# Kernel optimization log

Hardware: AMD Instinct MI355X
Metric: run time of the kernel (lower is better)

Reference implementation:

```python
import jax, jax.numpy as jnp
import numpy as np

# Config from VoVNetBEVTransformer: D=41, C=128, downsample=16, final_dim=(128,352)
B, N, C = 4, 6, 128
D, FH, FW = 41, 8, 22
OGH, OGW = 128, 352
XB = (-50.0, 50.0, 0.5)
YB = (-50.0, 50.0, 0.5)
ZB = (-10.0, 10.0, 20.0)
DBOUND = (4.0, 45.0, 1.0)
NX = int((XB[1] - XB[0]) / XB[2])  # 200
NY = int((YB[1] - YB[0]) / YB[2])  # 200
NZ = int((ZB[1] - ZB[0]) / ZB[2])  # 1


def _grid():
    dx = jnp.array([XB[2], YB[2], ZB[2]], jnp.float32)
    bx = jnp.array([XB[0] + XB[2] / 2.0, YB[0] + YB[2] / 2.0, ZB[0] + ZB[2] / 2.0], jnp.float32)
    return dx, bx


def _frustum():
    # (D, FH, FW, 3) grid of (u_pixel, v_pixel, depth) as in create_frustum
    ds = jnp.arange(DBOUND[0], DBOUND[1], DBOUND[2], dtype=jnp.float32)
    xs = jnp.linspace(0.0, OGW - 1.0, FW, dtype=jnp.float32)
    ys = jnp.linspace(0.0, OGH - 1.0, FH, dtype=jnp.float32)
    ds = jnp.broadcast_to(ds[:, None, None], (D, FH, FW))
    xs = jnp.broadcast_to(xs[None, None, :], (D, FH, FW))
    ys = jnp.broadcast_to(ys[None, :, None], (D, FH, FW))
    return jnp.stack([xs, ys, ds], axis=-1)


def setup_inputs() -> dict:
    key = jax.random.key(0)
    ks = jax.random.split(key, 6)
    cam_feats = jax.random.normal(ks[0], (B, N, D, FH, FW, C), jnp.float32)
    # cam-to-ego rotation: camera z (forward) -> ego x, plus small perturbation
    Rbase = jnp.array([[0.0, 0.0, 1.0], [-1.0, 0.0, 0.0], [0.0, -1.0, 0.0]], jnp.float32)
    rots = Rbase[None, None] + 0.02 * jax.random.normal(ks[1], (B, N, 3, 3), jnp.float32)
    trans = 1.5 * jax.random.normal(ks[2], (B, N, 3), jnp.float32)
    K = jnp.array([[500.0, 0.0, 176.0], [0.0, 500.0, 64.0], [0.0, 0.0, 1.0]], jnp.float32)
    intrins = K[None, None] + 0.5 * jax.random.normal(ks[3], (B, N, 3, 3), jnp.float32)
    post_rots = jnp.eye(3, dtype=jnp.float32)[None, None] + 0.01 * jax.random.normal(ks[4], (B, N, 3, 3), jnp.float32)
    post_trans = 0.5 * jax.random.normal(ks[5], (B, N, 3), jnp.float32)
    return {"cam_feats": cam_feats, "rots": rots, "trans": trans, "intrins": intrins,
            "post_rots": post_rots, "post_trans": post_trans}


def reference(cam_feats, rots, trans, intrins, post_rots, post_trans):
    dx, bx = _grid()
    frustum = _frustum()  # (D,FH,FW,3)
    # --- get_geometry ---
    pts = frustum[None, None] - post_trans[:, :, None, None, None, :]          # (B,N,D,FH,FW,3)
    pts = jnp.einsum('bnij,bndhwj->bndhwi', jnp.linalg.inv(post_rots), pts)
    pts = jnp.concatenate([pts[..., :2] * pts[..., 2:3], pts[..., 2:3]], axis=-1)
    combine = rots @ jnp.linalg.inv(intrins)
    pts = jnp.einsum('bnij,bndhwj->bndhwi', combine, pts) + trans[:, :, None, None, None, :]
    # --- voxel_pooling (QuickCumsum == segment-sum over voxel ranks) ---
    x = cam_feats.reshape(-1, C)                                               # (Nprime, C)
    g = ((pts - (bx - dx / 2.0)) / dx).astype(jnp.int32).reshape(-1, 3)        # trunc like torch .long()
    b_ix = jnp.repeat(jnp.arange(B, dtype=jnp.int32), N * D * FH * FW)
    kept = ((g[:, 0] >= 0) & (g[:, 0] < NX) & (g[:, 1] >= 0) & (g[:, 1] < NY)
            & (g[:, 2] >= 0) & (g[:, 2] < NZ))
    gc = jnp.clip(g, 0, jnp.array([NX - 1, NY - 1, NZ - 1], jnp.int32))
    S = NX * NY * NZ * B
    seg = ((gc[:, 0] * NY + gc[:, 1]) * NZ + gc[:, 2]) * B + b_ix              # same rank formula
    seg = jnp.where(kept, seg, S)                                              # dummy bin for dropped pts
    pooled = jax.ops.segment_sum(x, seg, num_segments=S + 1)[:S]               # (S, C)
    final = pooled.reshape(NX, NY, NZ, B, C).transpose(3, 2, 4, 0, 1)          # (B,NZ,C,NX,NY)
    return final.reshape(B, NZ * C, NX, NY)                                    # cat along z -> channels
```

## Files before the change

kernel.cpp:

```cpp
#include <hip/hip_runtime.h>

#define BATCH 4
#define NCAM  6
#define DNUM  41
#define FHN   8
#define FWN   22
#define CCH   128
#define NXV   200
#define NYV   200
#define NXY   40000
#define NPTS  173184

struct Mats {
    float iR[9];
    float comb[9];
    float tr[3];
    float pt[3];
};

__device__ void inv3x3_f32_gesv(const float* __restrict__ Ain, float* __restrict__ inv) {
#pragma clang fp contract(off)
    float A[9];
    for (int k = 0; k < 9; ++k) A[k] = Ain[k];
    int piv[3];
    for (int j = 0; j < 3; ++j) {
        int p = j;
        float amax = fabsf(A[j * 3 + j]);
        for (int i = j + 1; i < 3; ++i) {
            float v = fabsf(A[i * 3 + j]);
            if (v > amax) { amax = v; p = i; }
        }
        piv[j] = p;
        if (p != j)
            for (int k = 0; k < 3; ++k) { float t = A[j*3+k]; A[j*3+k] = A[p*3+k]; A[p*3+k] = t; }
        float rd = 1.0f / A[j * 3 + j];
        for (int i = j + 1; i < 3; ++i) A[i * 3 + j] = A[i * 3 + j] * rd;
        for (int i = j + 1; i < 3; ++i)
            for (int k = j + 1; k < 3; ++k)
                A[i * 3 + k] = A[i * 3 + k] - A[i * 3 + j] * A[j * 3 + k];
    }
    float rdiag[3] = {1.0f / A[0], 1.0f / A[4], 1.0f / A[8]};
    for (int c = 0; c < 3; ++c) {
        float b[3] = {0.0f, 0.0f, 0.0f};
        b[c] = 1.0f;
        for (int j = 0; j < 3; ++j) { int p = piv[j]; if (p != j) { float t = b[j]; b[j] = b[p]; b[p] = t; } }
        for (int k = 0; k < 3; ++k)
            for (int i = k + 1; i < 3; ++i)
                b[i] = b[i] - A[i * 3 + k] * b[k];
        for (int k = 2; k >= 0; --k) {
            b[k] = b[k] * rdiag[k];
            for (int i = 0; i < k; ++i)
                b[i] = b[i] - A[i * 3 + k] * b[k];
        }
        inv[0 + c] = b[0];
        inv[3 + c] = b[1];
        inv[6 + c] = b[2];
    }
}

__global__ void prep_kernel(const float* __restrict__ rots,
                            const float* __restrict__ trans,
                            const float* __restrict__ intrins,
                            const float* __restrict__ post_rots,
                            const float* __restrict__ post_trans,
                            Mats* __restrict__ mats) {
    int i = threadIdx.x;
    if (i >= BATCH * NCAM) return;
    Mats m;
    inv3x3_f32_gesv(post_rots + i * 9, m.iR);
    float invK[9];
    inv3x3_f32_gesv(intrins + i * 9, invK);
    {
#pragma clang fp contract(off)
        for (int r = 0; r < 3; ++r)
            for (int c = 0; c < 3; ++c) {
                float s = rots[i * 9 + r * 3 + 0] * invK[0 * 3 + c];
                s = s + rots[i * 9 + r * 3 + 1] * invK[1 * 3 + c];
                s = s + rots[i * 9 + r * 3 + 2] * invK[2 * 3 + c];
                m.comb[r * 3 + c] = s;
            }
    }
    for (int k = 0; k < 3; ++k) {
        m.tr[k] = trans[i * 3 + k];
        m.pt[k] = post_trans[i * 3 + k];
    }
    mats[i] = m;
}

__device__ __forceinline__ int point_voxel(int p, const Mats* __restrict__ mats) {
#pragma clang fp contract(off)
    int w = p % FWN;
    int t = p / FWN;
    int h = t % FHN;
    t /= FHN;
    int d = t % DNUM;
    t /= DNUM;
    int n = t % NCAM;
    int b = t / NCAM;

    const Mats m = mats[b * NCAM + n];

    float u   = (float)((double)w * (351.0 / 21.0));
    float v   = (float)((double)h * (127.0 / 7.0));
    float dep = 4.0f + (float)d;

    float p0 = u - m.pt[0];
    float p1 = v - m.pt[1];
    float p2 = dep - m.pt[2];
    float q0 = m.iR[0] * p0; q0 = q0 + m.iR[1] * p1; q0 = q0 + m.iR[2] * p2;
    float q1 = m.iR[3] * p0; q1 = q1 + m.iR[4] * p1; q1 = q1 + m.iR[5] * p2;
    float q2 = m.iR[6] * p0; q2 = q2 + m.iR[7] * p1; q2 = q2 + m.iR[8] * p2;
    float r0 = q0 * q2;
    float r1 = q1 * q2;
    float e0 = m.comb[0] * r0; e0 = e0 + m.comb[1] * r1; e0 = e0 + m.comb[2] * q2; e0 = e0 + m.tr[0];
    float e1 = m.comb[3] * r0; e1 = e1 + m.comb[4] * r1; e1 = e1 + m.comb[5] * q2; e1 = e1 + m.tr[1];
    float e2 = m.comb[6] * r0; e2 = e2 + m.comb[7] * r1; e2 = e2 + m.comb[8] * q2; e2 = e2 + m.tr[2];

    float gxf = (e0 + 50.0f) / 0.5f;
    float gyf = (e1 + 50.0f) / 0.5f;
    float gzf = (e2 + 10.0f) / 20.0f;
    int gx = (int)gxf;
    int gy = (int)gyf;
    int gz = (int)gzf;
    if (gx < 0 || gx >= NXV || gy < 0 || gy >= NYV || gz < 0 || gz >= 1) return -1;
    return b * NXY + gx * NYV + gy;
}

__global__ __launch_bounds__(128) void scatter_vox_kernel(const float* __restrict__ feats,
                                                          const Mats* __restrict__ mats,
                                                          float* __restrict__ vox) {
    int p = blockIdx.x;
    int vid = point_voxel(p, mats);
    if (vid < 0) return;
    int c = threadIdx.x;
    float f = feats[(size_t)p * CCH + c];
    atomicAdd(vox + (size_t)vid * CCH + c, f);
}

__global__ __launch_bounds__(256) void transpose_kernel(const float* __restrict__ vox,
                                                        float* __restrict__ out) {
    __shared__ float tile[32][33];
    int xy0 = blockIdx.x * 32;
    int c0  = blockIdx.y * 32;
    int b   = blockIdx.z;
    int tx = threadIdx.x, ty = threadIdx.y;
    const float* src = vox + (size_t)b * NXY * CCH;
#pragma unroll
    for (int j = 0; j < 32; j += 8)
        tile[ty + j][tx] = src[(size_t)(xy0 + ty + j) * CCH + (c0 + tx)];
    __syncthreads();
    float* dst = out + (size_t)b * CCH * NXY;
#pragma unroll
    for (int j = 0; j < 32; j += 8)
        dst[(size_t)(c0 + ty + j) * NXY + (xy0 + tx)] = tile[tx][ty + j];
}

__global__ __launch_bounds__(128) void scatter_direct_kernel(const float* __restrict__ feats,
                                                             const Mats* __restrict__ mats,
                                                             float* __restrict__ out) {
    int p = blockIdx.x;
    int vid = point_voxel(p, mats);
    if (vid < 0) return;
    int b  = vid / NXY;
    int xy = vid % NXY;
    int c = threadIdx.x;
    float f = feats[(size_t)p * CCH + c];
    atomicAdd(out + (size_t)(b * CCH + c) * NXY + xy, f);
}

extern "C" void kernel_launch(void* const* d_in, const int* in_sizes, int n_in,
                              void* d_out, int out_size, void* d_ws, size_t ws_size,
                              hipStream_t stream) {
    const float* cam_feats  = (const float*)d_in[0];
    const float* rots       = (const float*)d_in[1];
    const float* trans      = (const float*)d_in[2];
    const float* intrins    = (const float*)d_in[3];
    const float* post_rots  = (const float*)d_in[4];
    const float* post_trans = (const float*)d_in[5];
    float* out = (float*)d_out;
    Mats* mats = (Mats*)d_ws;

    prep_kernel<<<1, 64, 0, stream>>>(rots, trans, intrins, post_rots, post_trans, mats);

    const size_t vox_off   = 4096;
    const size_t vox_bytes = (size_t)BATCH * NXY * CCH * sizeof(float);

    if (ws_size >= vox_off + vox_bytes) {
        float* vox = (float*)((char*)d_ws + vox_off);
        hipMemsetAsync(vox, 0, vox_bytes, stream);
        scatter_vox_kernel<<<NPTS, CCH, 0, stream>>>(cam_feats, mats, vox);
        dim3 grid(NXY / 32, CCH / 32, BATCH);
        dim3 block(32, 8);
        transpose_kernel<<<grid, block, 0, stream>>>(vox, out);
    } else {
        hipMemsetAsync(d_out, 0, (size_t)out_size * sizeof(float), stream);
        scatter_direct_kernel<<<NPTS, CCH, 0, stream>>>(cam_feats, mats, out);
    }
}
```

Measured before the change: 229.9 us.

## Replace atomic scatter with counting-sort and per-voxel gather

Measured after the change: 462.0 us. 101% more time.

```diff
diff --git a/kernel.cpp b/kernel.cpp
--- a/kernel.cpp
+++ b/kernel.cpp
@@ -10,6 +10,9 @@
 #define NYV   200
 #define NXY   40000
 #define NPTS  173184
+#define SBINS (BATCH * NXY)
+#define SPAD  160256
+#define SCAN_BLOCKS 626
 
 struct Mats {
     float iR[9];
@@ -126,33 +129,109 @@
     return b * NXY + gx * NYV + gy;
 }
 
-__global__ __launch_bounds__(128) void scatter_vox_kernel(const float* __restrict__ feats,
-                                                          const Mats* __restrict__ mats,
-                                                          float* __restrict__ vox) {
-    int p = blockIdx.x;
+
+__global__ __launch_bounds__(256) void vid_kernel(const Mats* __restrict__ mats,
+                                                  int* __restrict__ vids,
+                                                  int* __restrict__ counts) {
+    int p = blockIdx.x * 256 + threadIdx.x;
+    if (p >= NPTS) return;
     int vid = point_voxel(p, mats);
-    if (vid < 0) return;
+    vids[p] = vid;
+    if (vid >= 0) atomicAdd(&counts[vid], 1);
+}
+
+__global__ __launch_bounds__(256) void scan_a(const int* __restrict__ counts,
+                                              int* __restrict__ offsets,
+                                              int* __restrict__ blockSums) {
+    __shared__ int buf[2][256];
+    int t = threadIdx.x;
+    int g = blockIdx.x * 256 + t;
+    int v = counts[g];
+    buf[0][t] = v;
+    __syncthreads();
+    int src = 0;
+    for (int off = 1; off < 256; off <<= 1) {
+        int val = buf[src][t];
+        if (t >= off) val += buf[src][t - off];
+        buf[src ^ 1][t] = val;
+        __syncthreads();
+        src ^= 1;
+    }
+    int incl = buf[src][t];
+    offsets[g] = incl - v;
+    if (t == 255) blockSums[blockIdx.x] = incl;
+}
+
+__global__ __launch_bounds__(1024) void scan_b(int* __restrict__ blockSums) {
+    __shared__ int buf[2][1024];
+    int t = threadIdx.x;
+    int v = (t < SCAN_BLOCKS) ? blockSums[t] : 0;
+    buf[0][t] = v;
+    __syncthreads();
+    int src = 0;
+    for (int off = 1; off < 1024; off <<= 1) {
+        int val = buf[src][t];
+        if (t >= off) val += buf[src][t - off];
+        buf[src ^ 1][t] = val;
+        __syncthreads();
+        src ^= 1;
+    }
+    int incl = buf[src][t];
+    if (t < SCAN_BLOCKS) blockSums[t] = incl - v;
+}
+
+__global__ __launch_bounds__(256) void scan_c(int* __restrict__ offsets,
+                                              const int* __restrict__ blockSums,
+                                              int* __restrict__ cursor) {
+    int g = blockIdx.x * 256 + threadIdx.x;
+    int v = offsets[g] + blockSums[blockIdx.x];
+    offsets[g] = v;
+    cursor[g] = v;
+}
+
+__global__ __launch_bounds__(256) void fill_kernel(const int* __restrict__ vids,
+                                                   int* __restrict__ cursor,
+                                                   int* __restrict__ plist) {
+    int p = blockIdx.x * 256 + threadIdx.x;
+    if (p >= NPTS) return;
+    int vid = vids[p];
+    if (vid >= 0) plist[atomicAdd(&cursor[vid], 1)] = p;
+}
+
+__global__ __launch_bounds__(128) void gather_kernel(const float* __restrict__ feats,
+                                                     const int* __restrict__ plist,
+                                                     const int* __restrict__ offsets,
+                                                     const int* __restrict__ counts,
+                                                     float* __restrict__ out) {
+    __shared__ float acc[32][129];
+    __shared__ int s_beg[32], s_cnt[32];
     int c = threadIdx.x;
-    float f = feats[(size_t)p * CCH + c];
-    atomicAdd(vox + (size_t)vid * CCH + c, f);
-}
-
-__global__ __launch_bounds__(256) void transpose_kernel(const float* __restrict__ vox,
-                                                        float* __restrict__ out) {
-    __shared__ float tile[32][33];
     int xy0 = blockIdx.x * 32;
-    int c0  = blockIdx.y * 32;
-    int b   = blockIdx.z;
-    int tx = threadIdx.x, ty = threadIdx.y;
-    const float* src = vox + (size_t)b * NXY * CCH;
-#pragma unroll
-    for (int j = 0; j < 32; j += 8)
-        tile[ty + j][tx] = src[(size_t)(xy0 + ty + j) * CCH + (c0 + tx)];
-    __syncthreads();
+    int b = blockIdx.y;
+    int bin0 = b * NXY + xy0;
+    if (c < 32) {
+        s_beg[c] = offsets[bin0 + c];
+        s_cnt[c] = counts[bin0 + c];
+    }
+    __syncthreads();
+    for (int j = 0; j < 32; ++j) {
+        int beg = s_beg[j];
+        int cnt = s_cnt[j];
+        float s = 0.0f;
+        for (int k = 0; k < cnt; ++k) {
+            int p = plist[beg + k];
+            s += feats[(size_t)p * CCH + c];
+        }
+        acc[j][c] = s;
+    }
+    __syncthreads();
+    int tx = c & 31, tg = c >> 5;
     float* dst = out + (size_t)b * CCH * NXY;
 #pragma unroll
-    for (int j = 0; j < 32; j += 8)
-        dst[(size_t)(c0 + ty + j) * NXY + (xy0 + tx)] = tile[tx][ty + j];
+    for (int cc = 0; cc < 32; ++cc) {
+        int ch = cc * 4 + tg;
+        dst[(size_t)ch * NXY + xy0 + tx] = acc[tx][ch];
+    }
 }
 
 __global__ __launch_bounds__(128) void scatter_direct_kernel(const float* __restrict__ feats,
@@ -182,16 +261,33 @@
 
     prep_kernel<<<1, 64, 0, stream>>>(rots, trans, intrins, post_rots, post_trans, mats);
 
-    const size_t vox_off   = 4096;
-    const size_t vox_bytes = (size_t)BATCH * NXY * CCH * sizeof(float);
-
-    if (ws_size >= vox_off + vox_bytes) {
-        float* vox = (float*)((char*)d_ws + vox_off);
-        hipMemsetAsync(vox, 0, vox_bytes, stream);
-        scatter_vox_kernel<<<NPTS, CCH, 0, stream>>>(cam_feats, mats, vox);
-        dim3 grid(NXY / 32, CCH / 32, BATCH);
-        dim3 block(32, 8);
-        transpose_kernel<<<grid, block, 0, stream>>>(vox, out);
+    const size_t OFF_VIDS    = 4096;
+    const size_t OFF_PLIST   = OFF_VIDS   + (size_t)NPTS * 4;
+    const size_t OFF_COUNTS  = OFF_PLIST  + (size_t)NPTS * 4;
+    const size_t OFF_OFFSETS = OFF_COUNTS + (size_t)SPAD * 4;
+    const size_t OFF_CURSOR  = OFF_OFFSETS+ (size_t)SPAD * 4;
+    const size_t OFF_BSUMS   = OFF_CURSOR + (size_t)SPAD * 4;
+    const size_t WS_NEEDED   = OFF_BSUMS + (size_t)SCAN_BLOCKS * 4;
+
+    if (ws_size >= WS_NEEDED) {
+        int* vids    = (int*)((char*)d_ws + OFF_VIDS);
+        int* plist   = (int*)((char*)d_ws + OFF_PLIST);
+        int* counts  = (int*)((char*)d_ws + OFF_COUNTS);
+        int* offsets = (int*)((char*)d_ws + OFF_OFFSETS);
+        int* cursor  = (int*)((char*)d_ws + OFF_CURSOR);
+        int* bsums   = (int*)((char*)d_ws + OFF_BSUMS);
+
+        hipMemsetAsync(counts, 0, (size_t)SPAD * 4, stream);
+
+        const int ptBlocks = (NPTS + 255) / 256;
+        vid_kernel<<<ptBlocks, 256, 0, stream>>>(mats, vids, counts);
+        scan_a<<<SCAN_BLOCKS, 256, 0, stream>>>(counts, offsets, bsums);
+        scan_b<<<1, 1024, 0, stream>>>(bsums);
+        scan_c<<<SCAN_BLOCKS, 256, 0, stream>>>(offsets, bsums, cursor);
+        fill_kernel<<<ptBlocks, 256, 0, stream>>>(vids, cursor, plist);
+
+        dim3 ggrid(NXY / 32, BATCH);
+        gather_kernel<<<ggrid, 128, 0, stream>>>(cam_feats, plist, offsets, counts, out);
     } else {
         hipMemsetAsync(d_out, 0, (size_t)out_size * sizeof(float), stream);
         scatter_direct_kernel<<<NPTS, CCH, 0, stream>>>(cam_feats, mats, out);
```

## Replace atomic voxel scatter and transpose with bucketed gather pooling

Applied to the files above, without the earlier changes.

Result: slower. 277.8 us (+20.8%).

```diff
diff --git a/kernel.cpp b/kernel.cpp
--- a/kernel.cpp
+++ b/kernel.cpp
@@ -10,6 +10,9 @@
 #define NYV   200
 #define NXY   40000
 #define NPTS  173184
+#define SBINS (BATCH * NXY)
+#define CAP   64
+#define OVF_MAX 8192
 
 struct Mats {
     float iR[9];
@@ -58,6 +61,32 @@
     }
 }
 
+__device__ void compute_mats(int i,
+                             const float* __restrict__ rots,
+                             const float* __restrict__ trans,
+                             const float* __restrict__ intrins,
+                             const float* __restrict__ post_rots,
+                             const float* __restrict__ post_trans,
+                             Mats* __restrict__ m) {
+    inv3x3_f32_gesv(post_rots + i * 9, m->iR);
+    float invK[9];
+    inv3x3_f32_gesv(intrins + i * 9, invK);
+    {
+#pragma clang fp contract(off)
+        for (int r = 0; r < 3; ++r)
+            for (int c = 0; c < 3; ++c) {
+                float s = rots[i * 9 + r * 3 + 0] * invK[0 * 3 + c];
+                s = s + rots[i * 9 + r * 3 + 1] * invK[1 * 3 + c];
+                s = s + rots[i * 9 + r * 3 + 2] * invK[2 * 3 + c];
+                m->comb[r * 3 + c] = s;
+            }
+    }
+    for (int k = 0; k < 3; ++k) {
+        m->tr[k] = trans[i * 3 + k];
+        m->pt[k] = post_trans[i * 3 + k];
+    }
+}
+
 __global__ void prep_kernel(const float* __restrict__ rots,
                             const float* __restrict__ trans,
                             const float* __restrict__ intrins,
@@ -67,23 +96,7 @@
     int i = threadIdx.x;
     if (i >= BATCH * NCAM) return;
     Mats m;
-    inv3x3_f32_gesv(post_rots + i * 9, m.iR);
-    float invK[9];
-    inv3x3_f32_gesv(intrins + i * 9, invK);
-    {
-#pragma clang fp contract(off)
-        for (int r = 0; r < 3; ++r)
-            for (int c = 0; c < 3; ++c) {
-                float s = rots[i * 9 + r * 3 + 0] * invK[0 * 3 + c];
-                s = s + rots[i * 9 + r * 3 + 1] * invK[1 * 3 + c];
-                s = s + rots[i * 9 + r * 3 + 2] * invK[2 * 3 + c];
-                m.comb[r * 3 + c] = s;
-            }
-    }
-    for (int k = 0; k < 3; ++k) {
-        m.tr[k] = trans[i * 3 + k];
-        m.pt[k] = post_trans[i * 3 + k];
-    }
+    compute_mats(i, rots, trans, intrins, post_rots, post_trans, &m);
     mats[i] = m;
 }
 
@@ -126,33 +139,104 @@
     return b * NXY + gx * NYV + gy;
 }
 
-__global__ __launch_bounds__(128) void scatter_vox_kernel(const float* __restrict__ feats,
-                                                          const Mats* __restrict__ mats,
-                                                          float* __restrict__ vox) {
-    int p = blockIdx.x;
-    int vid = point_voxel(p, mats);
+
+__global__ __launch_bounds__(256) void bucket_kernel(const float* __restrict__ rots,
+                                                     const float* __restrict__ trans,
+                                                     const float* __restrict__ intrins,
+                                                     const float* __restrict__ post_rots,
+                                                     const float* __restrict__ post_trans,
+                                                     int* __restrict__ counts,
+                                                     int* __restrict__ bucket,
+                                                     int* __restrict__ ovfcnt,
+                                                     int2* __restrict__ ovf) {
+    __shared__ Mats smats[BATCH * NCAM];
+    int t = threadIdx.x;
+    if (t < BATCH * NCAM) {
+        Mats m;
+        compute_mats(t, rots, trans, intrins, post_rots, post_trans, &m);
+        smats[t] = m;
+    }
+    __syncthreads();
+    int p = blockIdx.x * 256 + t;
+    if (p >= NPTS) return;
+    int vid = point_voxel(p, smats);
     if (vid < 0) return;
-    int c = threadIdx.x;
-    float f = feats[(size_t)p * CCH + c];
-    atomicAdd(vox + (size_t)vid * CCH + c, f);
-}
-
-__global__ __launch_bounds__(256) void transpose_kernel(const float* __restrict__ vox,
-                                                        float* __restrict__ out) {
-    __shared__ float tile[32][33];
+    int slot = atomicAdd(&counts[vid], 1);
+    if (slot < CAP) {
+        bucket[(size_t)vid * CAP + slot] = p;
+    } else {
+        int o = atomicAdd(ovfcnt, 1);
+        if (o < OVF_MAX) ovf[o] = make_int2(vid, p);
+    }
+}
+
+__global__ __launch_bounds__(256) void gather2_kernel(const float* __restrict__ feats,
+                                                      const int* __restrict__ counts,
+                                                      const int* __restrict__ bucket,
+                                                      const int* __restrict__ ovfcnt,
+                                                      const int2* __restrict__ ovf,
+                                                      float* __restrict__ out) {
+    __shared__ float acc[32][129];
+    int t = threadIdx.x;
+    int j = t >> 3;
+    int g = t & 7;
     int xy0 = blockIdx.x * 32;
-    int c0  = blockIdx.y * 32;
-    int b   = blockIdx.z;
-    int tx = threadIdx.x, ty = threadIdx.y;
-    const float* src = vox + (size_t)b * NXY * CCH;
+    int b = blockIdx.y;
+    int bin = b * NXY + xy0 + j;
+
+    int cntRaw = counts[bin];
+    int cnt = cntRaw < CAP ? cntRaw : CAP;
+
+    float4 a0 = {0.f,0.f,0.f,0.f}, a1 = a0, a2 = a0, a3 = a0;
+    const int* bk = bucket + (size_t)bin * CAP;
+    const float* fg = feats + g * 16;
+    for (int k = 0; k < cnt; ++k) {
+        int p = bk[k];
+        const float4* f4 = (const float4*)(fg + (size_t)p * CCH);
+        float4 v0 = f4[0], v1 = f4[1], v2 = f4[2], v3 = f4[3];
+        a0.x += v0.x; a0.y += v0.y; a0.z += v0.z; a0.w += v0.w;
+        a1.x += v1.x; a1.y += v1.y; a1.z += v1.z; a1.w += v1.w;
+        a2.x += v2.x; a2.y += v2.y; a2.z += v2.z; a2.w += v2.w;
+        a3.x += v3.x; a3.y += v3.y; a3.z += v3.z; a3.w += v3.w;
+    }
+    int novf = ovfcnt[0];
+    if (novf > 0) {
+        if (novf > OVF_MAX) novf = OVF_MAX;
+        for (int e = 0; e < novf; ++e) {
+            int2 vp = ovf[e];
+            if (vp.x == bin) {
+                const float4* f4 = (const float4*)(fg + (size_t)vp.y * CCH);
+                float4 v0 = f4[0], v1 = f4[1], v2 = f4[2], v3 = f4[3];
+                a0.x += v0.x; a0.y += v0.y; a0.z += v0.z; a0.w += v0.w;
+                a1.x += v1.x; a1.y += v1.y; a1.z += v1.z; a1.w += v1.w;
+                a2.x += v2.x; a2.y += v2.y; a2.z += v2.z; a2.w += v2.w;
+                a3.x += v3.x; a3.y += v3.y; a3.z += v3.z; a3.w += v3.w;
+            }
+        }
+    }
+
+    int nz = __syncthreads_count(cnt != 0);
+    int tx = t & 31, tg = t >> 5;
+    float* dst = out + (size_t)b * CCH * NXY + xy0 + tx;
+    if (nz == 0) {
 #pragma unroll
-    for (int j = 0; j < 32; j += 8)
-        tile[ty + j][tx] = src[(size_t)(xy0 + ty + j) * CCH + (c0 + tx)];
+        for (int cc = 0; cc < 16; ++cc)
+            dst[(size_t)(cc * 8 + tg) * NXY] = 0.0f;
+        return;
+    }
+
+    float* row = &acc[j][g * 16];
+    row[0]  = a0.x; row[1]  = a0.y; row[2]  = a0.z; row[3]  = a0.w;
+    row[4]  = a1.x; row[5]  = a1.y; row[6]  = a1.z; row[7]  = a1.w;
+    row[8]  = a2.x; row[9]  = a2.y; row[10] = a2.z; row[11] = a2.w;
+    row[12] = a3.x; row[13] = a3.y; row[14] = a3.z; row[15] = a3.w;
     __syncthreads();
-    float* dst = out + (size_t)b * CCH * NXY;
+
 #pragma unroll
-    for (int j = 0; j < 32; j += 8)
-        dst[(size_t)(c0 + ty + j) * NXY + (xy0 + tx)] = tile[tx][ty + j];
+    for (int cc = 0; cc < 16; ++cc) {
+        int ch = cc * 8 + tg;
+        dst[(size_t)ch * NXY] = acc[tx][ch];
+    }
 }
 
 __global__ __launch_bounds__(128) void scatter_direct_kernel(const float* __restrict__ feats,
@@ -178,21 +262,30 @@
     const float* post_rots  = (const float*)d_in[4];
     const float* post_trans = (const float*)d_in[5];
     float* out = (float*)d_out;
-    Mats* mats = (Mats*)d_ws;
-
-    prep_kernel<<<1, 64, 0, stream>>>(rots, trans, intrins, post_rots, post_trans, mats);
-
-    const size_t vox_off   = 4096;
-    const size_t vox_bytes = (size_t)BATCH * NXY * CCH * sizeof(float);
-
-    if (ws_size >= vox_off + vox_bytes) {
-        float* vox = (float*)((char*)d_ws + vox_off);
-        hipMemsetAsync(vox, 0, vox_bytes, stream);
-        scatter_vox_kernel<<<NPTS, CCH, 0, stream>>>(cam_feats, mats, vox);
-        dim3 grid(NXY / 32, CCH / 32, BATCH);
-        dim3 block(32, 8);
-        transpose_kernel<<<grid, block, 0, stream>>>(vox, out);
+
+    const size_t OFF_COUNTS = 4096;
+    const size_t OFF_OVFCNT = OFF_COUNTS + (size_t)SBINS * 4;
+    const size_t OFF_OVF    = OFF_OVFCNT + 256;
+    const size_t OFF_BUCKET = OFF_OVF + (size_t)OVF_MAX * 8;
+    const size_t WS_NEEDED  = OFF_BUCKET + (size_t)SBINS * CAP * 4;
+
+    if (ws_size >= WS_NEEDED) {
+        int*  counts = (int*)((char*)d_ws + OFF_COUNTS);
+        int*  ovfcnt = (int*)((char*)d_ws + OFF_OVFCNT);
+        int2* ovf    = (int2*)((char*)d_ws + OFF_OVF);
+        int*  bucket = (int*)((char*)d_ws + OFF_BUCKET);
+
+        hipMemsetAsync(counts, 0, (size_t)SBINS * 4 + 256, stream);
+
+        const int ptBlocks = (NPTS + 255) / 256;
+        bucket_kernel<<<ptBlocks, 256, 0, stream>>>(rots, trans, intrins, post_rots,
+                                                    post_trans, counts, bucket, ovfcnt, ovf);
+
+        dim3 ggrid(NXY / 32, BATCH);
+        gather2_kernel<<<ggrid, 256, 0, stream>>>(cam_feats, counts, bucket, ovfcnt, ovf, out);
     } else {
+        Mats* mats = (Mats*)d_ws;
+        prep_kernel<<<1, 64, 0, stream>>>(rots, trans, intrins, post_rots, post_trans, mats);
         hipMemsetAsync(d_out, 0, (size_t)out_size * sizeof(float), stream);
         scatter_direct_kernel<<<NPTS, CCH, 0, stream>>>(cam_feats, mats, out);
     }
```
